# Kernel tuning notes

Hardware: AMD Instinct MI355X
Metric: run time of the kernel (lower is better)

## Reference

```python
import jax, jax.numpy as jnp
import numpy as np

LENA, BATCH, ARR, HID = 8, 128, 1024, 64


def setup_inputs() -> dict:
    key = jax.random.key(0)
    ks = jax.random.split(key, 7)
    s = 0.1  # keep gates out of saturation
    return {
        "x": jax.random.normal(ks[0], (BATCH, ARR, 1), jnp.float32),
        "hn": jnp.zeros((LENA, BATCH, HID), jnp.float32),  # per-LSTM h0 (torch (1,B,H) squeezed)
        "Wih": jax.random.normal(ks[1], (LENA, 4 * HID, 1), jnp.float32) * s,
        "Whh": jax.random.normal(ks[2], (LENA, 4 * HID, HID), jnp.float32) * s,
        "bih": jax.random.normal(ks[3], (LENA, 4 * HID), jnp.float32) * s,
        "bhh": jax.random.normal(ks[4], (LENA, 4 * HID), jnp.float32) * s,
        "Wl": jax.random.normal(ks[5], (LENA, ARR), jnp.float32) * s,
        "bl": jax.random.normal(ks[6], (LENA,), jnp.float32) * s,
    }


def _ensemble_lstm_last_unit(x, hn, Wih, Whh, bias):
    # x: (B, T); hn: (L, B, H). All L LSTMs run fused in one scan over time.
    L, B, H = hn.shape
    c0 = jnp.zeros_like(hn)

    def step(carry, x_t):  # x_t: (B,)
        h, c = carry  # (L, B, H)
        gates = (x_t[None, :, None] * Wih[:, None, :, 0]
                 + jnp.einsum('lbh,lgh->lbg', h, Whh)
                 + bias[:, None, :])  # (L, B, 4H)
        i, f, g, o = jnp.split(gates, 4, axis=-1)  # torch gate order i,f,g,o
        i, f, o = jax.nn.sigmoid(i), jax.nn.sigmoid(f), jax.nn.sigmoid(o)
        c = f * c + i * jnp.tanh(g)
        h = o * jnp.tanh(c)
        return (h, c), h[:, :, -1]  # emit last hidden unit: o[:, :, -1]

    _, ys = jax.lax.scan(step, (hn, c0), x.T)  # ys: (T, L, B)
    return ys


def reference(x, hn, Wih, Whh, bih, bhh, Wl, bl):
    bias = bih + bhh  # (L, 4H)
    ys = _ensemble_lstm_last_unit(x[:, :, 0], hn, Wih, Whh, bias)  # (T, L, B)
    r = ys.sum(axis=1).T  # sum over ensemble -> (B, T=arr_size)
    return r @ Wl.T + bl  # (B, lenA)
```

## Files before the change

### kernel.cpp

```cpp
#include <hip/hip_runtime.h>


#define LENA 8
#define NB 128
#define NT 1024
#define NH 64

typedef __attribute__((ext_vector_type(4))) float f32x4;
typedef __attribute__((ext_vector_type(8))) short bf16x8;

__device__ __forceinline__ short f2bf(float f) {
    unsigned u = __float_as_uint(f);
    unsigned r = (u + 0x7FFFu + ((u >> 16) & 1u)) >> 16;
    return (short)r;
}

__global__ __launch_bounds__(256, 1) void lstm_v8_kernel(
    const float* __restrict__ x, const float* __restrict__ hn,
    const float* __restrict__ Wih, const float* __restrict__ Whh,
    const float* __restrict__ bih, const float* __restrict__ bhh,
    const float* __restrict__ Wl, float* __restrict__ ws)
{
    __shared__ float x4[NT][4];
    __shared__ float ring[NT][4];
    __shared__ __align__(16) short hbuf[2][32][8];

    const int tid = threadIdx.x;
    const int w   = tid >> 6;
    const int l   = tid & 63;
    const int col = l & 15;
    const int kg  = l >> 4;
    const int li  = blockIdx.x >> 5;
    const int bg  = blockIdx.x & 31;
    const int b0  = bg * 4;

    for (int i = tid; i < 4 * NT; i += 256) {
        int bb = i >> 10, t = i & (NT - 1);
        x4[t][bb] = x[(size_t)(b0 + bb) * NT + t];
    }
    {
        int b = tid >> 6, u = tid & 63;
        float v = hn[((size_t)li * NB + b0 + b) * NH + u];
        int slot = b * 8 + ((u >> 3) ^ (2 * b));
        hbuf[0][slot][u & 7] = f2bf(v);
    }

    const float RLN2 = 1.44269504f;
    bf16x8 bf[4][2];
    #pragma unroll
    for (int g = 0; g < 4; ++g) {
        const float sc = (g == 2) ? 2.0f * RLN2 : RLN2;
        const float* rp = Whh + ((size_t)li * 256 + 64 * g + 16 * w + col) * 64 + kg * 8;
        #pragma unroll
        for (int kh = 0; kh < 2; ++kh) {
            const float* q = rp + kh * 32;
            bf16x8 f;
            #pragma unroll
            for (int e = 0; e < 8; ++e) f[e] = f2bf(sc * q[e]);
            bf[g][kh] = f;
        }
    }
    const int u_c = 16 * w + col;
    float wih4[4];
    f32x4 cinit[4];
    #pragma unroll
    for (int g = 0; g < 4; ++g) {
        const float sc = (g == 2) ? 2.0f * RLN2 : RLN2;
        int rowc = li * 256 + 64 * g + u_c;
        wih4[g] = sc * Wih[rowc];
        float bv = sc * (bih[rowc] + bhh[rowc]);
        cinit[g][0] = bv; cinit[g][1] = bv; cinit[g][2] = bv; cinit[g][3] = bv;
    }

    const int b_r = col & 3;
    const int s0 = b_r * 8 + (kg ^ (2 * b_r));
    const int s1 = b_r * 8 + ((4 + kg) ^ (2 * b_r));
    const int wslot = kg * 8 + (((u_c >> 3)) ^ (2 * kg));
    const int wpos  = u_c & 7;
    const bool isring = (u_c == 63);

    const bool s_lo = (kg & 1) != 0;
    const bool s_hi = (kg & 2) != 0;
    float cst = 0.0f;

    __syncthreads();

    #pragma unroll 2
    for (int t = 0; t < NT; ++t) {
        const int p = t & 1;
        bf16x8 a0 = *(const bf16x8*)&hbuf[p][s0][0];
        bf16x8 a1 = *(const bf16x8*)&hbuf[p][s1][0];
        const float xsel = x4[t][kg];

        f32x4 acc[4];
        #pragma unroll
        for (int g = 0; g < 4; ++g) {
            f32x4 a = __builtin_amdgcn_mfma_f32_16x16x32_bf16(a0, bf[g][0], cinit[g], 0, 0, 0);
            acc[g] = __builtin_amdgcn_mfma_f32_16x16x32_bf16(a1, bf[g][1], a, 0, 0, 0);
        }

        float gs[4];
        #pragma unroll
        for (int g = 0; g < 4; ++g) {
            float va = s_lo ? acc[g][1] : acc[g][0];
            float vb = s_lo ? acc[g][3] : acc[g][2];
            gs[g] = s_hi ? vb : va;
        }

        float gi = fmaf(xsel, wih4[0], gs[0]);
        float gf = fmaf(xsel, wih4[1], gs[1]);
        float gg = fmaf(xsel, wih4[2], gs[2]);
        float go = fmaf(xsel, wih4[3], gs[3]);

        float iv = __builtin_amdgcn_rcpf(1.0f + __builtin_amdgcn_exp2f(-gi));
        float fv = __builtin_amdgcn_rcpf(1.0f + __builtin_amdgcn_exp2f(-gf));
        float gt = fmaf(-2.0f, __builtin_amdgcn_rcpf(1.0f + __builtin_amdgcn_exp2f(gg)), 1.0f);
        float ov = __builtin_amdgcn_rcpf(1.0f + __builtin_amdgcn_exp2f(-go));
        cst = fmaf(fv, cst, iv * gt);
        float ct = fmaf(-2.0f, __builtin_amdgcn_rcpf(1.0f + __builtin_amdgcn_exp2f(2.88539008f * cst)), 1.0f);
        float hh = ov * ct;

        hbuf[p ^ 1][wslot][wpos] = f2bf(hh);
        if (isring) ring[t][kg] = hh;
        __syncthreads();
    }

    {
        const int b = w;
        const int a = l & 7, ch = l >> 3;
        const float* wlp = Wl + (size_t)a * NT + ch * 128;
        const float* rg  = &ring[ch * 128][0];
        float pacc = 0.0f;
        #pragma unroll 4
        for (int i = 0; i < 128; ++i)
            pacc = fmaf(rg[i * 4 + b], wlp[i], pacc);
        pacc += __shfl_xor(pacc, 8);
        pacc += __shfl_xor(pacc, 16);
        pacc += __shfl_xor(pacc, 32);
        if (l < 8) ws[(size_t)blockIdx.x * 32 + b * 8 + a] = pacc;
    }
}

__global__ __launch_bounds__(256) void reduce_kernel(
    const float* __restrict__ ws, const float* __restrict__ bl, float* __restrict__ out)
{
    int tid = blockIdx.x * 256 + threadIdx.x;
    if (tid >= NB * LENA) return;
    int b = tid >> 3, a = tid & 7;
    int bg = b >> 2, bb = b & 3;
    float s = bl[a];
    #pragma unroll
    for (int li = 0; li < LENA; ++li)
        s += ws[((size_t)(li * 32 + bg)) * 32 + bb * 8 + a];
    out[tid] = s;
}

extern "C" void kernel_launch(void* const* d_in, const int* in_sizes, int n_in,
                              void* d_out, int out_size, void* d_ws, size_t ws_size,
                              hipStream_t stream) {
    const float* x   = (const float*)d_in[0];
    const float* hn  = (const float*)d_in[1];
    const float* Wih = (const float*)d_in[2];
    const float* Whh = (const float*)d_in[3];
    const float* bih = (const float*)d_in[4];
    const float* bhh = (const float*)d_in[5];
    const float* Wl  = (const float*)d_in[6];
    const float* bl  = (const float*)d_in[7];
    float* out = (float*)d_out;
    float* ws  = (float*)d_ws;

    lstm_v8_kernel<<<dim3(256), dim3(256), 0, stream>>>(x, hn, Wih, Whh, bih, bhh, Wl, ws);
    reduce_kernel<<<dim3(4), dim3(256), 0, stream>>>(ws, bl, out);
}
```

Before: 279.3 us.

## Split batch into 2-row groups per block, doubling grid to 512 blocks

Each block now handles 2 batch rows instead of 4, so the grid grows from 256 to 512 blocks and launch bounds allow 2 blocks per CU. Only half the lanes do the cell update and the MFMA tile is half-used. The goal is to fill all CUs, since the serial recurrence makes per-step latency the limit. The cost is wasted MFMA rows and some change to the final projection, reduction and workspace layout.

```diff
diff --git a/kernel.cpp b/kernel.cpp
--- a/kernel.cpp
+++ b/kernel.cpp
@@ -15,30 +15,31 @@
     return (short)r;
 }
 
-__global__ __launch_bounds__(256, 1) void lstm_v8_kernel(
+__global__ __launch_bounds__(256, 2) void lstm_v9_kernel(
     const float* __restrict__ x, const float* __restrict__ hn,
     const float* __restrict__ Wih, const float* __restrict__ Whh,
     const float* __restrict__ bih, const float* __restrict__ bhh,
     const float* __restrict__ Wl, float* __restrict__ ws)
 {
-    __shared__ float x4[NT][4];
-    __shared__ float ring[NT][4];
-    __shared__ __align__(16) short hbuf[2][32][8];
+    __shared__ float x2[NT][2];
+    __shared__ float ring[NT][2];
+    __shared__ __align__(16) short hbuf[2][16][8];
+    __shared__ float pws[2][2][8];
 
     const int tid = threadIdx.x;
     const int w   = tid >> 6;
     const int l   = tid & 63;
     const int col = l & 15;
     const int kg  = l >> 4;
-    const int li  = blockIdx.x >> 5;
-    const int bg  = blockIdx.x & 31;
-    const int b0  = bg * 4;
+    const int li  = blockIdx.x >> 6;
+    const int bg  = blockIdx.x & 63;
+    const int b0  = bg * 2;
 
-    for (int i = tid; i < 4 * NT; i += 256) {
+    for (int i = tid; i < 2 * NT; i += 256) {
         int bb = i >> 10, t = i & (NT - 1);
-        x4[t][bb] = x[(size_t)(b0 + bb) * NT + t];
+        x2[t][bb] = x[(size_t)(b0 + bb) * NT + t];
     }
-    {
+    if (tid < 128) {
         int b = tid >> 6, u = tid & 63;
         float v = hn[((size_t)li * NB + b0 + b) * NH + u];
         int slot = b * 8 + ((u >> 3) ^ (2 * b));
@@ -72,15 +73,15 @@
         cinit[g][0] = bv; cinit[g][1] = bv; cinit[g][2] = bv; cinit[g][3] = bv;
     }
 
-    const int b_r = col & 3;
+    const int b_r = col & 1;
     const int s0 = b_r * 8 + (kg ^ (2 * b_r));
     const int s1 = b_r * 8 + ((4 + kg) ^ (2 * b_r));
-    const int wslot = kg * 8 + (((u_c >> 3)) ^ (2 * kg));
+    const int wslot = kg * 8 + ((u_c >> 3) ^ (2 * kg));
     const int wpos  = u_c & 7;
-    const bool isring = (u_c == 63);
+    const bool docell = (kg < 2);
+    const bool isring = (u_c == 63) && docell;
 
     const bool s_lo = (kg & 1) != 0;
-    const bool s_hi = (kg & 2) != 0;
     float cst = 0.0f;
 
     __syncthreads();
@@ -90,7 +91,6 @@
         const int p = t & 1;
         bf16x8 a0 = *(const bf16x8*)&hbuf[p][s0][0];
         bf16x8 a1 = *(const bf16x8*)&hbuf[p][s1][0];
-        const float xsel = x4[t][kg];
 
         f32x4 acc[4];
         #pragma unroll
@@ -99,45 +99,50 @@
             acc[g] = __builtin_amdgcn_mfma_f32_16x16x32_bf16(a1, bf[g][1], a, 0, 0, 0);
         }
 
-        float gs[4];
-        #pragma unroll
-        for (int g = 0; g < 4; ++g) {
-            float va = s_lo ? acc[g][1] : acc[g][0];
-            float vb = s_lo ? acc[g][3] : acc[g][2];
-            gs[g] = s_hi ? vb : va;
+        if (docell) {
+            const float xsel = x2[t][kg];
+            float gs0 = s_lo ? acc[0][1] : acc[0][0];
+            float gs1 = s_lo ? acc[1][1] : acc[1][0];
+            float gs2 = s_lo ? acc[2][1] : acc[2][0];
+            float gs3 = s_lo ? acc[3][1] : acc[3][0];
+
+            float gi = fmaf(xsel, wih4[0], gs0);
+            float gf = fmaf(xsel, wih4[1], gs1);
+            float gg = fmaf(xsel, wih4[2], gs2);
+            float go = fmaf(xsel, wih4[3], gs3);
+
+            float iv = __builtin_amdgcn_rcpf(1.0f + __builtin_amdgcn_exp2f(-gi));
+            float fv = __builtin_amdgcn_rcpf(1.0f + __builtin_amdgcn_exp2f(-gf));
+            float gt = fmaf(-2.0f, __builtin_amdgcn_rcpf(1.0f + __builtin_amdgcn_exp2f(gg)), 1.0f);
+            float ov = __builtin_amdgcn_rcpf(1.0f + __builtin_amdgcn_exp2f(-go));
+            cst = fmaf(fv, cst, iv * gt);
+            float ct = fmaf(-2.0f, __builtin_amdgcn_rcpf(1.0f + __builtin_amdgcn_exp2f(2.88539008f * cst)), 1.0f);
+            float hh = ov * ct;
+
+            hbuf[p ^ 1][wslot][wpos] = f2bf(hh);
+            if (isring) ring[t][kg] = hh;
         }
-
-        float gi = fmaf(xsel, wih4[0], gs[0]);
-        float gf = fmaf(xsel, wih4[1], gs[1]);
-        float gg = fmaf(xsel, wih4[2], gs[2]);
-        float go = fmaf(xsel, wih4[3], gs[3]);
-
-        float iv = __builtin_amdgcn_rcpf(1.0f + __builtin_amdgcn_exp2f(-gi));
-        float fv = __builtin_amdgcn_rcpf(1.0f + __builtin_amdgcn_exp2f(-gf));
-        float gt = fmaf(-2.0f, __builtin_amdgcn_rcpf(1.0f + __builtin_amdgcn_exp2f(gg)), 1.0f);
-        float ov = __builtin_amdgcn_rcpf(1.0f + __builtin_amdgcn_exp2f(-go));
-        cst = fmaf(fv, cst, iv * gt);
-        float ct = fmaf(-2.0f, __builtin_amdgcn_rcpf(1.0f + __builtin_amdgcn_exp2f(2.88539008f * cst)), 1.0f);
-        float hh = ov * ct;
-
-        hbuf[p ^ 1][wslot][wpos] = f2bf(hh);
-        if (isring) ring[t][kg] = hh;
         __syncthreads();
     }
 
     {
-        const int b = w;
+        const int b = w >> 1, p2 = w & 1;
         const int a = l & 7, ch = l >> 3;
-        const float* wlp = Wl + (size_t)a * NT + ch * 128;
-        const float* rg  = &ring[ch * 128][0];
+        const int tb = p2 * 512 + ch * 64;
+        const float* wlp = Wl + (size_t)a * NT + tb;
         float pacc = 0.0f;
         #pragma unroll 4
-        for (int i = 0; i < 128; ++i)
-            pacc = fmaf(rg[i * 4 + b], wlp[i], pacc);
+        for (int i = 0; i < 64; ++i)
+            pacc = fmaf(ring[tb + i][b], wlp[i], pacc);
         pacc += __shfl_xor(pacc, 8);
         pacc += __shfl_xor(pacc, 16);
         pacc += __shfl_xor(pacc, 32);
-        if (l < 8) ws[(size_t)blockIdx.x * 32 + b * 8 + a] = pacc;
+        if (l < 8) pws[b][p2][a] = pacc;
+    }
+    __syncthreads();
+    if (tid < 16) {
+        int b = tid >> 3, a = tid & 7;
+        ws[((size_t)blockIdx.x * 2 + b) * 8 + a] = pws[b][0][a] + pws[b][1][a];
     }
 }
 
@@ -147,11 +152,11 @@
     int tid = blockIdx.x * 256 + threadIdx.x;
     if (tid >= NB * LENA) return;
     int b = tid >> 3, a = tid & 7;
-    int bg = b >> 2, bb = b & 3;
+    int bg = b >> 1, bb = b & 1;
     float s = bl[a];
     #pragma unroll
     for (int li = 0; li < LENA; ++li)
-        s += ws[((size_t)(li * 32 + bg)) * 32 + bb * 8 + a];
+        s += ws[(((size_t)li * 64 + bg) * 2 + bb) * 8 + a];
     out[tid] = s;
 }
 
@@ -169,6 +174,6 @@
     float* out = (float*)d_out;
     float* ws  = (float*)d_ws;
 
-    lstm_v8_kernel<<<dim3(256), dim3(256), 0, stream>>>(x, hn, Wih, Whh, bih, bhh, Wl, ws);
+    lstm_v9_kernel<<<dim3(512), dim3(256), 0, stream>>>(x, hn, Wih, Whh, bih, bhh, Wl, ws);
     reduce_kernel<<<dim3(4), dim3(256), 0, stream>>>(ws, bl, out);
 }
```

Measured after the change: 287.5 us. 1.03x slower.

## Split batch into two groups and ping-pong MFMA with gate math

Applied to the files above, without the earlier changes.

The four batch rows per block are split into two independent pairs (A and B). Each half-step issues the MFMAs for one pair while running the elementwise gate and cell update for the other pair's previous MFMA results, so matrix and vector work overlap across the recurrence dependency. The aim is to hide MFMA latency and the transcendental chain within each barrier interval. The cost is two barriers per timestep instead of one, and each MFMA now covers only two useful rows.

```diff
diff --git a/kernel.cpp b/kernel.cpp
--- a/kernel.cpp
+++ b/kernel.cpp
@@ -15,7 +15,7 @@
     return (short)r;
 }
 
-__global__ __launch_bounds__(256, 1) void lstm_v8_kernel(
+__global__ __launch_bounds__(256, 1) void lstm_v11_kernel(
     const float* __restrict__ x, const float* __restrict__ hn,
     const float* __restrict__ Wih, const float* __restrict__ Whh,
     const float* __restrict__ bih, const float* __restrict__ bhh,
@@ -23,26 +23,30 @@
 {
     __shared__ float x4[NT][4];
     __shared__ float ring[NT][4];
-    __shared__ __align__(16) short hbuf[2][32][8];
+    __shared__ __align__(16) short hA[16][8];
+    __shared__ __align__(16) short hB[16][8];
 
     const int tid = threadIdx.x;
     const int w   = tid >> 6;
     const int l   = tid & 63;
     const int col = l & 15;
     const int kg  = l >> 4;
+    const int bb  = kg & 1;
     const int li  = blockIdx.x >> 5;
     const int bg  = blockIdx.x & 31;
     const int b0  = bg * 4;
 
     for (int i = tid; i < 4 * NT; i += 256) {
-        int bb = i >> 10, t = i & (NT - 1);
-        x4[t][bb] = x[(size_t)(b0 + bb) * NT + t];
+        int bx = i >> 10, t = i & (NT - 1);
+        x4[t][bx] = x[(size_t)(b0 + bx) * NT + t];
     }
     {
-        int b = tid >> 6, u = tid & 63;
-        float v = hn[((size_t)li * NB + b0 + b) * NH + u];
-        int slot = b * 8 + ((u >> 3) ^ (2 * b));
-        hbuf[0][slot][u & 7] = f2bf(v);
+        int bsel = tid >> 6, u = tid & 63;
+        float v = hn[((size_t)li * NB + b0 + bsel) * NH + u];
+        int bbs = bsel & 1;
+        int slot = bbs * 8 + ((u >> 3) ^ (2 * bbs));
+        short hv = f2bf(v);
+        if (bsel < 2) hA[slot][u & 7] = hv; else hB[slot][u & 7] = hv;
     }
 
     const float RLN2 = 1.44269504f;
@@ -72,56 +76,78 @@
         cinit[g][0] = bv; cinit[g][1] = bv; cinit[g][2] = bv; cinit[g][3] = bv;
     }
 
-    const int b_r = col & 3;
+    const int b_r = col & 1;
     const int s0 = b_r * 8 + (kg ^ (2 * b_r));
     const int s1 = b_r * 8 + ((4 + kg) ^ (2 * b_r));
-    const int wslot = kg * 8 + (((u_c >> 3)) ^ (2 * kg));
+    const int wslot = bb * 8 + ((u_c >> 3) ^ (2 * bb));
     const int wpos  = u_c & 7;
     const bool isring = (u_c == 63);
 
-    const bool s_lo = (kg & 1) != 0;
-    const bool s_hi = (kg & 2) != 0;
-    float cst = 0.0f;
+    float cstA = 0.0f, cstB = 0.0f;
+    f32x4 accA[4], accB[4];
 
     __syncthreads();
 
-    #pragma unroll 2
-    for (int t = 0; t < NT; ++t) {
-        const int p = t & 1;
-        bf16x8 a0 = *(const bf16x8*)&hbuf[p][s0][0];
-        bf16x8 a1 = *(const bf16x8*)&hbuf[p][s1][0];
-        const float xsel = x4[t][kg];
-
-        f32x4 acc[4];
+    {
+        bf16x8 a0 = *(const bf16x8*)&hB[s0][0];
+        bf16x8 a1 = *(const bf16x8*)&hB[s1][0];
         #pragma unroll
         for (int g = 0; g < 4; ++g) {
             f32x4 a = __builtin_amdgcn_mfma_f32_16x16x32_bf16(a0, bf[g][0], cinit[g], 0, 0, 0);
-            acc[g] = __builtin_amdgcn_mfma_f32_16x16x32_bf16(a1, bf[g][1], a, 0, 0, 0);
-        }
-
-        float gs[4];
-        #pragma unroll
-        for (int g = 0; g < 4; ++g) {
-            float va = s_lo ? acc[g][1] : acc[g][0];
-            float vb = s_lo ? acc[g][3] : acc[g][2];
-            gs[g] = s_hi ? vb : va;
-        }
-
-        float gi = fmaf(xsel, wih4[0], gs[0]);
-        float gf = fmaf(xsel, wih4[1], gs[1]);
-        float gg = fmaf(xsel, wih4[2], gs[2]);
-        float go = fmaf(xsel, wih4[3], gs[3]);
-
-        float iv = __builtin_amdgcn_rcpf(1.0f + __builtin_amdgcn_exp2f(-gi));
-        float fv = __builtin_amdgcn_rcpf(1.0f + __builtin_amdgcn_exp2f(-gf));
-        float gt = fmaf(-2.0f, __builtin_amdgcn_rcpf(1.0f + __builtin_amdgcn_exp2f(gg)), 1.0f);
-        float ov = __builtin_amdgcn_rcpf(1.0f + __builtin_amdgcn_exp2f(-go));
-        cst = fmaf(fv, cst, iv * gt);
-        float ct = fmaf(-2.0f, __builtin_amdgcn_rcpf(1.0f + __builtin_amdgcn_exp2f(2.88539008f * cst)), 1.0f);
-        float hh = ov * ct;
-
-        hbuf[p ^ 1][wslot][wpos] = f2bf(hh);
-        if (isring) ring[t][kg] = hh;
+            accB[g] = __builtin_amdgcn_mfma_f32_16x16x32_bf16(a1, bf[g][1], a, 0, 0, 0);
+        }
+    }
+    __syncthreads();
+
+    #pragma unroll 1
+    for (int t = 0; t < NT; ++t) {
+        {
+            bf16x8 a0 = *(const bf16x8*)&hA[s0][0];
+            bf16x8 a1 = *(const bf16x8*)&hA[s1][0];
+            #pragma unroll
+            for (int g = 0; g < 4; ++g) {
+                f32x4 a = __builtin_amdgcn_mfma_f32_16x16x32_bf16(a0, bf[g][0], cinit[g], 0, 0, 0);
+                accA[g] = __builtin_amdgcn_mfma_f32_16x16x32_bf16(a1, bf[g][1], a, 0, 0, 0);
+            }
+            const float xv = x4[t][2 + bb];
+            float gi = fmaf(xv, wih4[0], bb ? accB[0][1] : accB[0][0]);
+            float gf = fmaf(xv, wih4[1], bb ? accB[1][1] : accB[1][0]);
+            float gg = fmaf(xv, wih4[2], bb ? accB[2][1] : accB[2][0]);
+            float go = fmaf(xv, wih4[3], bb ? accB[3][1] : accB[3][0]);
+            float iv = __builtin_amdgcn_rcpf(1.0f + __builtin_amdgcn_exp2f(-gi));
+            float fv = __builtin_amdgcn_rcpf(1.0f + __builtin_amdgcn_exp2f(-gf));
+            float gt = fmaf(-2.0f, __builtin_amdgcn_rcpf(1.0f + __builtin_amdgcn_exp2f(gg)), 1.0f);
+            float ov = __builtin_amdgcn_rcpf(1.0f + __builtin_amdgcn_exp2f(-go));
+            cstB = fmaf(fv, cstB, iv * gt);
+            float ct = fmaf(-2.0f, __builtin_amdgcn_rcpf(1.0f + __builtin_amdgcn_exp2f(2.88539008f * cstB)), 1.0f);
+            float hh = ov * ct;
+            hB[wslot][wpos] = f2bf(hh);
+            if (isring) ring[t][2 + bb] = hh;
+        }
+        __syncthreads();
+        {
+            bf16x8 a0 = *(const bf16x8*)&hB[s0][0];
+            bf16x8 a1 = *(const bf16x8*)&hB[s1][0];
+            #pragma unroll
+            for (int g = 0; g < 4; ++g) {
+                f32x4 a = __builtin_amdgcn_mfma_f32_16x16x32_bf16(a0, bf[g][0], cinit[g], 0, 0, 0);
+                accB[g] = __builtin_amdgcn_mfma_f32_16x16x32_bf16(a1, bf[g][1], a, 0, 0, 0);
+            }
+            const float xv = x4[t][bb];
+            float gi = fmaf(xv, wih4[0], bb ? accA[0][1] : accA[0][0]);
+            float gf = fmaf(xv, wih4[1], bb ? accA[1][1] : accA[1][0]);
+            float gg = fmaf(xv, wih4[2], bb ? accA[2][1] : accA[2][0]);
+            float go = fmaf(xv, wih4[3], bb ? accA[3][1] : accA[3][0]);
+            float iv = __builtin_amdgcn_rcpf(1.0f + __builtin_amdgcn_exp2f(-gi));
+            float fv = __builtin_amdgcn_rcpf(1.0f + __builtin_amdgcn_exp2f(-gf));
+            float gt = fmaf(-2.0f, __builtin_amdgcn_rcpf(1.0f + __builtin_amdgcn_exp2f(gg)), 1.0f);
+            float ov = __builtin_amdgcn_rcpf(1.0f + __builtin_amdgcn_exp2f(-go));
+            cstA = fmaf(fv, cstA, iv * gt);
+            float ct = fmaf(-2.0f, __builtin_amdgcn_rcpf(1.0f + __builtin_amdgcn_exp2f(2.88539008f * cstA)), 1.0f);
+            float hh = ov * ct;
+            hA[wslot][wpos] = f2bf(hh);
+            if (isring) ring[t][bb] = hh;
+        }
         __syncthreads();
     }
 
@@ -147,11 +173,11 @@
     int tid = blockIdx.x * 256 + threadIdx.x;
     if (tid >= NB * LENA) return;
     int b = tid >> 3, a = tid & 7;
-    int bg = b >> 2, bb = b & 3;
+    int bg = b >> 2, bx = b & 3;
     float s = bl[a];
     #pragma unroll
     for (int li = 0; li < LENA; ++li)
-        s += ws[((size_t)(li * 32 + bg)) * 32 + bb * 8 + a];
+        s += ws[((size_t)(li * 32 + bg)) * 32 + bx * 8 + a];
     out[tid] = s;
 }
 
@@ -169,6 +195,6 @@
     float* out = (float*)d_out;
     float* ws  = (float*)d_ws;
 
-    lstm_v8_kernel<<<dim3(256), dim3(256), 0, stream>>>(x, hn, Wih, Whh, bih, bhh, Wl, ws);
+    lstm_v11_kernel<<<dim3(256), dim3(256), 0, stream>>>(x, hn, Wih, Whh, bih, bhh, Wl, ws);
     reduce_kernel<<<dim3(4), dim3(256), 0, stream>>>(ws, bl, out);
 }
```

New measurement: 471.0 us. 1.69x slower.
